# Kernel optimization log

Measured on AMD Instinct MI355X. Metric: run time of the kernel, lower is better.

## Reference

```python
import jax, jax.numpy as jnp
import numpy as np

B, S, D, H = 4, 2048, 1024, 16
DK = D // H

def setup_inputs() -> dict:
    key = jax.random.key(0)
    ks = jax.random.split(key, 11)
    s = 1.0 / np.sqrt(D)
    return {
        "query": jax.random.normal(ks[0], (B, S, D), jnp.float32),
        "key_": jax.random.normal(ks[1], (B, S, D), jnp.float32),
        "value": jax.random.normal(ks[2], (B, S, D), jnp.float32),
        "Wq": jax.random.uniform(ks[3], (D, D), jnp.float32, -s, s),
        "bq": jax.random.uniform(ks[4], (D,), jnp.float32, -s, s),
        "Wk": jax.random.uniform(ks[5], (D, D), jnp.float32, -s, s),
        "bk": jax.random.uniform(ks[6], (D,), jnp.float32, -s, s),
        "Wv": jax.random.uniform(ks[7], (D, D), jnp.float32, -s, s),
        "bv": jax.random.uniform(ks[8], (D,), jnp.float32, -s, s),
        "Wo": jax.random.uniform(ks[9], (D, D), jnp.float32, -s, s),
        "bo": jax.random.uniform(ks[10], (D,), jnp.float32, -s, s),
    }

def _split_heads(x):
    # [B,S,D] -> [B,H,S,DK]
    b, s, _ = x.shape
    return x.reshape(b, s, H, DK).transpose(0, 2, 1, 3)

def reference(query, key_, value, Wq, bq, Wk, bk, Wv, bv, Wo, bo):
    Q = _split_heads(query @ Wq.T + bq)
    K = _split_heads(key_ @ Wk.T + bk)
    V = _split_heads(value @ Wv.T + bv)
    scores = jnp.einsum('bhqd,bhkd->bhqk', Q, K) / np.sqrt(DK).astype(np.float32)
    attn = jax.nn.softmax(scores, axis=-1)
    ctx = jnp.einsum('bhqk,bhkd->bhqd', attn, V)  # [B,H,S,DK]
    ctx = ctx.transpose(0, 2, 1, 3).reshape(query.shape[0], -1, D)
    return ctx @ Wo.T + bo
```

## Files before the change

### kernel.cpp

```cpp
#include <hip/hip_runtime.h>
#include <hip/hip_bf16.h>
#include <math.h>


#define B_SZ   4
#define S_LEN  2048
#define D_DIM  1024
#define NH     16
#define DKD    64
#define M_TOT  (B_SZ * S_LEN)

typedef __bf16 bf16_t;
typedef bf16_t bf16x8 __attribute__((ext_vector_type(8)));
typedef bf16_t bf16x4 __attribute__((ext_vector_type(4)));
typedef float  f32x4  __attribute__((ext_vector_type(4)));

typedef __attribute__((address_space(1))) void gvoid;
typedef __attribute__((address_space(3))) void lvoid;

extern "C" __device__ float __ocml_native_exp2_f32(float);

__global__ __launch_bounds__(256)
void cvt3_kernel(const float* __restrict__ s0, const float* __restrict__ s1,
                 const float* __restrict__ s2, bf16_t* __restrict__ d0,
                 bf16_t* __restrict__ d1, bf16_t* __restrict__ d2, int n4)
{
    const float* src = (blockIdx.z == 0) ? s0 : (blockIdx.z == 1) ? s1 : s2;
    bf16_t*      dst = (blockIdx.z == 0) ? d0 : (blockIdx.z == 1) ? d1 : d2;
    const int i = blockIdx.x * blockDim.x + threadIdx.x;
    if (i < n4) {
        f32x4 v = *(const f32x4*)(src + (size_t)i * 4);
        bf16x4 o;
        #pragma unroll
        for (int j = 0; j < 4; ++j) o[j] = (bf16_t)v[j];
        *(bf16x4*)(dst + (size_t)i * 4) = o;
    }
}

__global__ __launch_bounds__(256)
void cvt_kernel(const float* __restrict__ src, bf16_t* __restrict__ dst, int n4)
{
    const int i = blockIdx.x * blockDim.x + threadIdx.x;
    if (i < n4) {
        f32x4 v = *(const f32x4*)(src + (size_t)i * 4);
        bf16x4 o;
        #pragma unroll
        for (int j = 0; j < 4; ++j) o[j] = (bf16_t)v[j];
        *(bf16x4*)(dst + (size_t)i * 4) = o;
    }
}

__global__ __launch_bounds__(256, 2)
void qkv_gemm(const float* __restrict__ Aq, const float* __restrict__ Ak,
              const float* __restrict__ Av,
              const bf16_t* __restrict__ Wqb, const bf16_t* __restrict__ Wkb,
              const bf16_t* __restrict__ Wvb,
              const float* __restrict__ bq, const float* __restrict__ bk,
              const float* __restrict__ bv,
              bf16_t* __restrict__ Qw, bf16_t* __restrict__ Kw,
              bf16_t* __restrict__ Vt, float qscale)
{
    constexpr int K = 1024, N = 1024;
    constexpr int BM = 128, BK = 64;

    __shared__ __align__(16) bf16_t lA[2][BM * 32];
    __shared__ __align__(16) bf16_t lB[2][128 * 32];

    const int z = blockIdx.z;
    const float* A  = (z == 0) ? Aq : (z == 1) ? Ak : Av;
    const bf16_t* W = (z == 0) ? Wqb : (z == 1) ? Wkb : Wvb;
    const float* bias = (z == 0) ? bq : (z == 1) ? bk : bv;
    const float scale = (z == 0) ? qscale : 1.0f;

    const int tid  = threadIdx.x;
    const int wave = tid >> 6;
    const int lane = tid & 63;

    const int row0 = blockIdx.x * BM;
    const int col0 = blockIdx.y * 128;

    const int wr = (wave >> 1) * 64;
    const int wc = (wave & 1) * 64;

    f32x4 acc[4][4] = {};

    const int frow = lane & 15;
    const int kq   = (lane >> 4) * 8;

    const int arow = tid >> 3;
    const int ak8  = (tid & 7) * 8;
    const int asub = (tid >> 2) & 1;
    const int akk  = (tid & 3) * 8;

    f32x4 pa[4][2];
    #pragma unroll
    for (int p = 0; p < 4; ++p) {
        const float* g = A + (size_t)(row0 + p * 32 + arow) * K + ak8;
        pa[p][0] = *(const f32x4*)g;
        pa[p][1] = *(const f32x4*)(g + 4);
    }

    for (int k0 = 0; k0 < K; k0 += BK) {
        __syncthreads();
        #pragma unroll
        for (int p = 0; p < 4; ++p) {
            bf16x8 a8;
            #pragma unroll
            for (int j = 0; j < 4; ++j) {
                a8[j]     = (bf16_t)pa[p][0][j];
                a8[4 + j] = (bf16_t)pa[p][1][j];
            }
            *(bf16x8*)(&lA[asub][(p * 32 + arow) * 32 + akk]) = a8;
        }
        #pragma unroll
        for (int s = 0; s < 2; ++s)
            #pragma unroll
            for (int c = 0; c < 2; ++c) {
                const int chunk = c * 4 + wave;
                const int e     = chunk * 512 + lane * 8;
                const int rr    = e >> 5;
                const int kk    = e & 31;
                __builtin_amdgcn_global_load_lds(
                    (gvoid*)(W + (size_t)(col0 + rr) * K + k0 + 32 * s + kk),
                    (lvoid*)(&lB[s][chunk * 512]), 16, 0, 0);
            }
        __syncthreads();

        if (k0 + BK < K) {
            #pragma unroll
            for (int p = 0; p < 4; ++p) {
                const float* g = A + (size_t)(row0 + p * 32 + arow) * K + (k0 + BK) + ak8;
                pa[p][0] = *(const f32x4*)g;
                pa[p][1] = *(const f32x4*)(g + 4);
            }
        }

        #pragma unroll
        for (int s = 0; s < 2; ++s) {
            bf16x8 af[4], bfr[4];
            #pragma unroll
            for (int i = 0; i < 4; ++i) {
                af[i]  = *(const bf16x8*)(&lA[s][(wr + i * 16 + frow) * 32 + kq]);
                bfr[i] = *(const bf16x8*)(&lB[s][(wc + i * 16 + frow) * 32 + kq]);
            }
            #pragma unroll
            for (int i = 0; i < 4; ++i)
                #pragma unroll
                for (int j = 0; j < 4; ++j)
                    acc[i][j] = __builtin_amdgcn_mfma_f32_16x16x32_bf16(af[i], bfr[j], acc[i][j], 0, 0, 0);
        }
    }

    const int rb   = (lane >> 4) * 4;
    const int ccol = lane & 15;
    #pragma unroll
    for (int j = 0; j < 4; ++j) {
        const int n = col0 + wc + j * 16 + ccol;
        const float bvv = bias[n];
        #pragma unroll
        for (int i = 0; i < 4; ++i) {
            const int m = row0 + wr + i * 16 + rb;
            if (z == 2) {
                bf16x4 o4;
                #pragma unroll
                for (int r = 0; r < 4; ++r) o4[r] = (bf16_t)(acc[i][j][r] + bvv);
                *(bf16x4*)(Vt + (size_t)n * M_TOT + m) = o4;
            } else {
                bf16_t* Cp = (z == 0) ? Qw : Kw;
                #pragma unroll
                for (int r = 0; r < 4; ++r)
                    Cp[(size_t)(m + r) * N + n] = (bf16_t)((acc[i][j][r] + bvv) * scale);
            }
        }
    }
}

__global__ __launch_bounds__(256, 2)
void gemm_out(const bf16_t* __restrict__ A, const bf16_t* __restrict__ Bt,
              const float* __restrict__ bias, float* __restrict__ C)
{
    constexpr int K = 1024, N = 1024;
    constexpr int BM = 128, BK = 64;

    __shared__ __align__(16) bf16_t lA[2][BM * 32];
    __shared__ __align__(16) bf16_t lB[2][128 * 32];

    const int tid  = threadIdx.x;
    const int wave = tid >> 6;
    const int lane = tid & 63;

    const int row0 = blockIdx.x * BM;
    const int col0 = blockIdx.y * 128;

    const int wr = (wave >> 1) * 64;
    const int wc = (wave & 1) * 64;

    f32x4 acc[4][4] = {};

    const int frow = lane & 15;
    const int kq   = (lane >> 4) * 8;

    for (int k0 = 0; k0 < K; k0 += BK) {
        __syncthreads();
        #pragma unroll
        for (int s = 0; s < 2; ++s)
            #pragma unroll
            for (int c = 0; c < 2; ++c) {
                const int chunk = c * 4 + wave;
                const int e     = chunk * 512 + lane * 8;
                const int r     = e >> 5;
                const int kk    = e & 31;
                __builtin_amdgcn_global_load_lds(
                    (gvoid*)(A + (size_t)(row0 + r) * K + k0 + 32 * s + kk),
                    (lvoid*)(&lA[s][chunk * 512]), 16, 0, 0);
                __builtin_amdgcn_global_load_lds(
                    (gvoid*)(Bt + (size_t)(col0 + r) * K + k0 + 32 * s + kk),
                    (lvoid*)(&lB[s][chunk * 512]), 16, 0, 0);
            }
        __syncthreads();

        #pragma unroll
        for (int s = 0; s < 2; ++s) {
            bf16x8 af[4], bfr[4];
            #pragma unroll
            for (int i = 0; i < 4; ++i) {
                af[i]  = *(const bf16x8*)(&lA[s][(wr + i * 16 + frow) * 32 + kq]);
                bfr[i] = *(const bf16x8*)(&lB[s][(wc + i * 16 + frow) * 32 + kq]);
            }
            #pragma unroll
            for (int i = 0; i < 4; ++i)
                #pragma unroll
                for (int j = 0; j < 4; ++j)
                    acc[i][j] = __builtin_amdgcn_mfma_f32_16x16x32_bf16(af[i], bfr[j], acc[i][j], 0, 0, 0);
        }
    }

    const int rb   = (lane >> 4) * 4;
    const int ccol = lane & 15;
    #pragma unroll
    for (int j = 0; j < 4; ++j) {
        const int n = col0 + wc + j * 16 + ccol;
        const float bvv = bias[n];
        #pragma unroll
        for (int i = 0; i < 4; ++i) {
            const int m = row0 + wr + i * 16 + rb;
            #pragma unroll
            for (int r = 0; r < 4; ++r)
                C[(size_t)(m + r) * N + n] = acc[i][j][r] + bvv;
        }
    }
}

__global__ __launch_bounds__(256, 2)
void attn_mfma(const bf16_t* __restrict__ Qg, const bf16_t* __restrict__ Kg,
               const bf16_t* __restrict__ Vt, bf16_t* __restrict__ ctx)
{
    constexpr int PSTR = 72;
    __shared__ __align__(16) bf16_t lK[64 * PSTR];
    __shared__ __align__(16) bf16_t lV[64 * PSTR];
    __shared__ __align__(16) bf16_t lP[4][64 * PSTR];

    const int tid  = threadIdx.x;
    const int wave = tid >> 6;
    const int lane = tid & 63;
    const int qd   = lane >> 4;
    const int c    = lane & 15;

    const int g    = blockIdx.x;
    const int bh   = ((g >> 6) << 3) | (g & 7);
    const int qblk = (g >> 3) & 7;
    const int b    = bh >> 4;
    const int h    = bh & 15;

    const int q0 = qblk * 256 + wave * 64;

    const bf16_t* Qb = Qg + ((size_t)(b * S_LEN + q0)) * D_DIM + h * DKD;
    const bf16_t* Kb = Kg + ((size_t)(b * S_LEN)) * D_DIM + h * DKD;
    const bf16_t* Vb = Vt + ((size_t)(h * DKD)) * M_TOT + b * S_LEN;

    bf16_t* Pw = &lP[wave][0];

    bf16x8 qf[4][2];
    #pragma unroll
    for (int qt = 0; qt < 4; ++qt)
        #pragma unroll
        for (int ks = 0; ks < 2; ++ks)
            qf[qt][ks] = *(const bf16x8*)(Qb + (size_t)(qt * 16 + c) * D_DIM + ks * 32 + qd * 8);

    bf16x8 ones;
    #pragma unroll
    for (int i = 0; i < 8; ++i) ones[i] = (bf16_t)1.0f;

    f32x4 oacc[4][4] = {};
    f32x4 lacc[4]    = {};

    const int srow = tid >> 3;
    const int sc8  = (tid & 7) * 8;

    bf16x8 kv[2], vv[2];
    #pragma unroll
    for (int cc = 0; cc < 2; ++cc) {
        const int row = cc * 32 + srow;
        kv[cc] = *(const bf16x8*)(Kb + (size_t)row * D_DIM + sc8);
        vv[cc] = *(const bf16x8*)(Vb + (size_t)row * M_TOT + sc8);
    }

    for (int kt = 0; kt < S_LEN; kt += 64) {
        __syncthreads();
        #pragma unroll
        for (int cc = 0; cc < 2; ++cc) {
            const int row = cc * 32 + srow;
            *(bf16x8*)(lK + row * PSTR + sc8) = kv[cc];
            *(bf16x8*)(lV + row * PSTR + sc8) = vv[cc];
        }
        __syncthreads();

        if (kt + 64 < S_LEN) {
            #pragma unroll
            for (int cc = 0; cc < 2; ++cc) {
                const int row = cc * 32 + srow;
                kv[cc] = *(const bf16x8*)(Kb + (size_t)(kt + 64 + row) * D_DIM + sc8);
                vv[cc] = *(const bf16x8*)(Vb + (size_t)row * M_TOT + kt + 64 + sc8);
            }
        }

        bf16x8 kf[4][2];
        #pragma unroll
        for (int i = 0; i < 4; ++i)
            #pragma unroll
            for (int ks = 0; ks < 2; ++ks)
                kf[i][ks] = *(const bf16x8*)(lK + (i * 16 + c) * PSTR + ks * 32 + qd * 8);

        #pragma unroll
        for (int qh = 0; qh < 2; ++qh) {
            f32x4 st[4][2] = {};
            __builtin_amdgcn_s_setprio(1);
            #pragma unroll
            for (int ks = 0; ks < 2; ++ks)
                #pragma unroll
                for (int i = 0; i < 4; ++i)
                    #pragma unroll
                    for (int qt = 0; qt < 2; ++qt)
                        st[i][qt] = __builtin_amdgcn_mfma_f32_16x16x32_bf16(
                            kf[i][ks], qf[qh * 2 + qt][ks], st[i][qt], 0, 0, 0);
            __builtin_amdgcn_s_setprio(0);

            #pragma unroll
            for (int i = 0; i < 4; ++i)
                #pragma unroll
                for (int qt = 0; qt < 2; ++qt) {
                    bf16x4 pw;
                    #pragma unroll
                    for (int r = 0; r < 4; ++r)
                        pw[r] = (bf16_t)__ocml_native_exp2_f32(st[i][qt][r]);
                    *(bf16x4*)(Pw + ((qh * 2 + qt) * 16 + c) * PSTR + i * 16 + qd * 4) = pw;
                }
        }

        bf16x8 vf[4][2];
        #pragma unroll
        for (int fm = 0; fm < 4; ++fm)
            #pragma unroll
            for (int ks = 0; ks < 2; ++ks)
                vf[fm][ks] = *(const bf16x8*)(lV + (fm * 16 + c) * PSTR + ks * 32 + qd * 8);

        __builtin_amdgcn_s_setprio(1);
        #pragma unroll
        for (int qn = 0; qn < 4; ++qn)
            #pragma unroll
            for (int ks = 0; ks < 2; ++ks) {
                bf16x8 pf = *(const bf16x8*)(Pw + (qn * 16 + c) * PSTR + ks * 32 + qd * 8);
                lacc[qn] = __builtin_amdgcn_mfma_f32_16x16x32_bf16(ones, pf, lacc[qn], 0, 0, 0);
                #pragma unroll
                for (int fm = 0; fm < 4; ++fm)
                    oacc[fm][qn] = __builtin_amdgcn_mfma_f32_16x16x32_bf16(vf[fm][ks], pf, oacc[fm][qn], 0, 0, 0);
            }
        __builtin_amdgcn_s_setprio(0);
    }

    #pragma unroll
    for (int qn = 0; qn < 4; ++qn) {
        const float linv = 1.0f / lacc[qn][0];
        bf16_t* op = ctx + ((size_t)(b * S_LEN + q0 + qn * 16 + c)) * D_DIM + h * DKD + qd * 4;
        #pragma unroll
        for (int fm = 0; fm < 4; ++fm) {
            bf16x4 o4;
            #pragma unroll
            for (int r = 0; r < 4; ++r) o4[r] = (bf16_t)(oacc[fm][qn][r] * linv);
            *(bf16x4*)(op + fm * 16) = o4;
        }
    }
}

extern "C" void kernel_launch(void* const* d_in, const int* in_sizes, int n_in,
                              void* d_out, int out_size, void* d_ws, size_t ws_size,
                              hipStream_t stream)
{
    const float* query = (const float*)d_in[0];
    const float* key_  = (const float*)d_in[1];
    const float* value = (const float*)d_in[2];
    const float* Wq    = (const float*)d_in[3];
    const float* bq    = (const float*)d_in[4];
    const float* Wk    = (const float*)d_in[5];
    const float* bk    = (const float*)d_in[6];
    const float* Wv    = (const float*)d_in[7];
    const float* bv    = (const float*)d_in[8];
    const float* Wo    = (const float*)d_in[9];
    const float* bo    = (const float*)d_in[10];
    float* out = (float*)d_out;

    const size_t mat  = (size_t)M_TOT * D_DIM;
    const size_t wmat = (size_t)D_DIM * D_DIM;

    bf16_t* t0 = (bf16_t*)d_ws;
    bf16_t* w0 = t0 + mat;
    bf16_t* Qw = w0 + wmat;
    bf16_t* Kw = Qw + mat;
    bf16_t* Vt = Kw + mat;
    bf16_t* w1 = t0;
    bf16_t* w2 = t0 + wmat;

    const int gcvt_w = (int)(wmat / 4 / 256);
    const float qscale = 0.18033688011112042f;

    cvt3_kernel<<<dim3(gcvt_w, 1, 3), 256, 0, stream>>>(Wq, Wk, Wv, w0, w1, w2,
                                                        (int)(wmat / 4));

    qkv_gemm<<<dim3(M_TOT / 128, D_DIM / 128, 3), 256, 0, stream>>>(
        query, key_, value, w0, w1, w2, bq, bk, bv, Qw, Kw, Vt, qscale);

    cvt_kernel<<<gcvt_w, 256, 0, stream>>>(Wo, w0, (int)(wmat / 4));

    attn_mfma<<<dim3(B_SZ * NH * (S_LEN / 256)), 256, 0, stream>>>(Qw, Kw, Vt, t0);

    gemm_out<<<dim3(M_TOT / 128, D_DIM / 128), 256, 0, stream>>>(t0, w0, bo, out);
}
```

Measured before the change: 330.0 us.

## Double-buffer LDS weight tiles in QKV and output GEMMs with async prefetch

Both projection GEMMs now keep two LDS buffers for the streamed global_load_lds tiles. The next k-tile is issued before computing the current one, and manual s_waitcnt vmcnt counts plus raw s_barrier replace the full __syncthreads drain. The aim is to hide global-to-LDS latency behind the MFMA work. In exchange LDS use grows, and the qkv launch bounds go up to 3 blocks per CU, which may push up register pressure. Correctness depends on the hand-picked vmcnt values matching the number of loads in flight, including the register prefetch of A in qkv_gemm.

```diff
diff --git a/kernel.cpp b/kernel.cpp
--- a/kernel.cpp
+++ b/kernel.cpp
@@ -50,7 +50,7 @@
     }
 }
 
-__global__ __launch_bounds__(256, 2)
+__global__ __launch_bounds__(256, 3)
 void qkv_gemm(const float* __restrict__ Aq, const float* __restrict__ Ak,
               const float* __restrict__ Av,
               const bf16_t* __restrict__ Wqb, const bf16_t* __restrict__ Wkb,
@@ -62,9 +62,10 @@
 {
     constexpr int K = 1024, N = 1024;
     constexpr int BM = 128, BK = 64;
+    constexpr int NT = K / BK;
 
     __shared__ __align__(16) bf16_t lA[2][BM * 32];
-    __shared__ __align__(16) bf16_t lB[2][128 * 32];
+    __shared__ __align__(16) bf16_t lB[2][2][128 * 32];
 
     const int z = blockIdx.z;
     const float* A  = (z == 0) ? Aq : (z == 1) ? Ak : Av;
@@ -92,6 +93,23 @@
     const int asub = (tid >> 2) & 1;
     const int akk  = (tid & 3) * 8;
 
+    auto stageB = [&](int k0s, int bufi) {
+        #pragma unroll
+        for (int s = 0; s < 2; ++s)
+            #pragma unroll
+            for (int c2 = 0; c2 < 2; ++c2) {
+                const int chunk = c2 * 4 + wave;
+                const int e     = chunk * 512 + lane * 8;
+                const int rr    = e >> 5;
+                const int kk    = e & 31;
+                __builtin_amdgcn_global_load_lds(
+                    (gvoid*)(W + (size_t)(col0 + rr) * K + k0s + 32 * s + kk),
+                    (lvoid*)(&lB[bufi][s][chunk * 512]), 16, 0, 0);
+            }
+    };
+
+    stageB(0, 0);
+
     f32x4 pa[4][2];
     #pragma unroll
     for (int p = 0; p < 4; ++p) {
@@ -100,8 +118,12 @@
         pa[p][1] = *(const f32x4*)(g + 4);
     }
 
-    for (int k0 = 0; k0 < K; k0 += BK) {
-        __syncthreads();
+    for (int t = 0; t < NT; ++t) {
+        const int k0  = t * BK;
+        const int buf = t & 1;
+
+        if (t + 1 < NT) stageB(k0 + BK, buf ^ 1);
+
         #pragma unroll
         for (int p = 0; p < 4; ++p) {
             bf16x8 a8;
@@ -112,21 +134,14 @@
             }
             *(bf16x8*)(&lA[asub][(p * 32 + arow) * 32 + akk]) = a8;
         }
-        #pragma unroll
-        for (int s = 0; s < 2; ++s)
-            #pragma unroll
-            for (int c = 0; c < 2; ++c) {
-                const int chunk = c * 4 + wave;
-                const int e     = chunk * 512 + lane * 8;
-                const int rr    = e >> 5;
-                const int kk    = e & 31;
-                __builtin_amdgcn_global_load_lds(
-                    (gvoid*)(W + (size_t)(col0 + rr) * K + k0 + 32 * s + kk),
-                    (lvoid*)(&lB[s][chunk * 512]), 16, 0, 0);
-            }
-        __syncthreads();
-
-        if (k0 + BK < K) {
+
+        if (t + 1 < NT)
+            asm volatile("s_waitcnt vmcnt(4) lgkmcnt(0)" ::: "memory");
+        else
+            asm volatile("s_waitcnt vmcnt(0) lgkmcnt(0)" ::: "memory");
+        __builtin_amdgcn_s_barrier();
+
+        if (t + 1 < NT) {
             #pragma unroll
             for (int p = 0; p < 4; ++p) {
                 const float* g = A + (size_t)(row0 + p * 32 + arow) * K + (k0 + BK) + ak8;
@@ -141,7 +156,7 @@
             #pragma unroll
             for (int i = 0; i < 4; ++i) {
                 af[i]  = *(const bf16x8*)(&lA[s][(wr + i * 16 + frow) * 32 + kq]);
-                bfr[i] = *(const bf16x8*)(&lB[s][(wc + i * 16 + frow) * 32 + kq]);
+                bfr[i] = *(const bf16x8*)(&lB[buf][s][(wc + i * 16 + frow) * 32 + kq]);
             }
             #pragma unroll
             for (int i = 0; i < 4; ++i)
@@ -149,6 +164,9 @@
                 for (int j = 0; j < 4; ++j)
                     acc[i][j] = __builtin_amdgcn_mfma_f32_16x16x32_bf16(af[i], bfr[j], acc[i][j], 0, 0, 0);
         }
+
+        asm volatile("" ::: "memory");
+        __builtin_amdgcn_s_barrier();
     }
 
     const int rb   = (lane >> 4) * 4;
@@ -181,9 +199,10 @@
 {
     constexpr int K = 1024, N = 1024;
     constexpr int BM = 128, BK = 64;
-
-    __shared__ __align__(16) bf16_t lA[2][BM * 32];
-    __shared__ __align__(16) bf16_t lB[2][128 * 32];
+    constexpr int NT = K / BK;
+
+    __shared__ __align__(16) bf16_t lA[2][2][BM * 32];
+    __shared__ __align__(16) bf16_t lB[2][2][128 * 32];
 
     const int tid  = threadIdx.x;
     const int wave = tid >> 6;
@@ -200,32 +219,44 @@
     const int frow = lane & 15;
     const int kq   = (lane >> 4) * 8;
 
-    for (int k0 = 0; k0 < K; k0 += BK) {
-        __syncthreads();
+    auto stage = [&](int k0s, int bufi) {
         #pragma unroll
         for (int s = 0; s < 2; ++s)
             #pragma unroll
-            for (int c = 0; c < 2; ++c) {
-                const int chunk = c * 4 + wave;
+            for (int c2 = 0; c2 < 2; ++c2) {
+                const int chunk = c2 * 4 + wave;
                 const int e     = chunk * 512 + lane * 8;
                 const int r     = e >> 5;
                 const int kk    = e & 31;
                 __builtin_amdgcn_global_load_lds(
-                    (gvoid*)(A + (size_t)(row0 + r) * K + k0 + 32 * s + kk),
-                    (lvoid*)(&lA[s][chunk * 512]), 16, 0, 0);
+                    (gvoid*)(A + (size_t)(row0 + r) * K + k0s + 32 * s + kk),
+                    (lvoid*)(&lA[bufi][s][chunk * 512]), 16, 0, 0);
                 __builtin_amdgcn_global_load_lds(
-                    (gvoid*)(Bt + (size_t)(col0 + r) * K + k0 + 32 * s + kk),
-                    (lvoid*)(&lB[s][chunk * 512]), 16, 0, 0);
-            }
-        __syncthreads();
+                    (gvoid*)(Bt + (size_t)(col0 + r) * K + k0s + 32 * s + kk),
+                    (lvoid*)(&lB[bufi][s][chunk * 512]), 16, 0, 0);
+            }
+    };
+
+    stage(0, 0);
+
+    for (int t = 0; t < NT; ++t) {
+        const int buf = t & 1;
+
+        if (t + 1 < NT) {
+            stage((t + 1) * BK, buf ^ 1);
+            asm volatile("s_waitcnt vmcnt(8)" ::: "memory");
+        } else {
+            asm volatile("s_waitcnt vmcnt(0)" ::: "memory");
+        }
+        __builtin_amdgcn_s_barrier();
 
         #pragma unroll
         for (int s = 0; s < 2; ++s) {
             bf16x8 af[4], bfr[4];
             #pragma unroll
             for (int i = 0; i < 4; ++i) {
-                af[i]  = *(const bf16x8*)(&lA[s][(wr + i * 16 + frow) * 32 + kq]);
-                bfr[i] = *(const bf16x8*)(&lB[s][(wc + i * 16 + frow) * 32 + kq]);
+                af[i]  = *(const bf16x8*)(&lA[buf][s][(wr + i * 16 + frow) * 32 + kq]);
+                bfr[i] = *(const bf16x8*)(&lB[buf][s][(wc + i * 16 + frow) * 32 + kq]);
             }
             #pragma unroll
             for (int i = 0; i < 4; ++i)
@@ -233,6 +264,9 @@
                 for (int j = 0; j < 4; ++j)
                     acc[i][j] = __builtin_amdgcn_mfma_f32_16x16x32_bf16(af[i], bfr[j], acc[i][j], 0, 0, 0);
         }
+
+        asm volatile("" ::: "memory");
+        __builtin_amdgcn_s_barrier();
     }
 
     const int rb   = (lane >> 4) * 4;
```

After: 330.9 us. About the same (+0.3%).
